# Performance work log

Measured on AMD Instinct MI355X. Metric: run time of the kernel, lower is better.

## Reference

```python
import jax, jax.numpy as jnp
import numpy as np

N = 100000      # nodes
E = 1200000     # edges
G = 2048        # graphs in batch
FIN, H, FOUT, K = 75, 16, 64, 3  # in/hidden/out channels, num_stacks


def setup_inputs() -> dict:
    key = jax.random.key(0)
    ks = jax.random.split(key, 12)
    s = 0.1
    return {
        "x": jax.random.normal(ks[0], (N, FIN), jnp.float32),
        "edge_index": jax.random.randint(ks[1], (2, E), 0, N),
        "batch": jnp.sort(jax.random.randint(ks[2], (N,), 0, G)),
        # ARMAConv1 (75 -> 16), shared weights across T=2 layers
        "w1_init": jax.random.normal(ks[3], (K, FIN, H), jnp.float32) * s,
        "w1_w": jax.random.normal(ks[4], (K, H, H), jnp.float32) * s,
        "w1_root": jax.random.normal(ks[5], (K, FIN, H), jnp.float32) * s,
        "w1_bias": jnp.zeros((K, 1, H), jnp.float32),
        # ARMAConv2 (16 -> 64), act=None
        "w2_init": jax.random.normal(ks[6], (K, H, FOUT), jnp.float32) * s,
        "w2_w": jax.random.normal(ks[7], (K, FOUT, FOUT), jnp.float32) * s,
        "w2_root": jax.random.normal(ks[8], (K, H, FOUT), jnp.float32) * s,
        "w2_bias": jnp.zeros((K, 1, FOUT), jnp.float32),
        # gather head Linear(64, 1)
        "wg": jax.random.normal(ks[9], (FOUT, 1), jnp.float32) * s,
        "bg": jnp.zeros((1,), jnp.float32),
    }


def reference(x, edge_index, batch, w1_init, w1_w, w1_root, w1_bias,
              w2_init, w2_w, w2_root, w2_bias, wg, bg):
    row, col = edge_index[0], edge_index[1]
    # gcn_norm without self-loops: deg over target nodes, sym normalization
    deg = jnp.zeros((N,), x.dtype).at[col].add(1.0)
    dinv = jnp.where(deg > 0, deg ** -0.5, 0.0)
    norm = dinv[row] * dinv[col]  # [E]

    def prop(h):  # h: [K, N, F] -> A_norm @ h per stack
        msg = h[:, row, :] * norm[None, :, None]        # [K, E, F]
        return jnp.zeros_like(h).at[:, col, :].add(msg)

    def arma(x0, wi, ww, wr, b, act):
        # x0: [N, Fin]; T=2 layers, shared weights
        out = None
        for t in range(2):
            if t == 0:
                out = jnp.einsum('nf,kfo->kno', x0, wi)   # init transform
            else:
                out = jnp.einsum('kno,kop->knp', out, ww)  # shared weight
            out = prop(out)
            out = out + jnp.einsum('nf,kfo->kno', x0, wr) + b  # root + bias
            if act:
                out = jax.nn.relu(out)
        return out.mean(axis=0)  # average over K stacks -> [N, F]

    h1 = jax.nn.relu(arma(x, w1_init, w1_w, w1_root, w1_bias, True))
    h2 = arma(h1, w2_init, w2_w, w2_root, w2_bias, False)
    # global_add_pool over graph ids, then linear head
    pooled = jnp.zeros((G, h2.shape[-1]), h2.dtype).at[batch].add(h2)
    return pooled @ wg + bg  # [G, 1]
```

## Files before the change

kernel.cpp:

```cpp
#include <hip/hip_runtime.h>

#define NN 100000
#define NE 1200000
#define NG 2048
#define NBK 391
#define CAPQ 4096
#define CAPE 5120

static inline int cdiv(long long a, int b) { return (int)((a + b - 1) / b); }

__device__ __forceinline__ unsigned short f2bf(float f) {
    unsigned int u = __float_as_uint(f);
    u += 0x7fffu + ((u >> 16) & 1u);
    return (unsigned short)(u >> 16);
}
__device__ __forceinline__ unsigned int pack2(float a, float b) {
    return (unsigned int)f2bf(a) | ((unsigned int)f2bf(b) << 16);
}
__device__ __forceinline__ float lo2f(unsigned int w) { return __uint_as_float(w << 16); }
__device__ __forceinline__ float hi2f(unsigned int w) { return __uint_as_float(w & 0xffff0000u); }

__global__ void k_init(int* __restrict__ gcur, uint4* __restrict__ A16,
                       uint4* __restrict__ B16, uint4* __restrict__ h1p16,
                       uint4* __restrict__ g1p16, float* __restrict__ dinv) {
    int g = blockIdx.x * blockDim.x + threadIdx.x;
    if (g < NBK) gcur[g] = g * CAPQ;
    if (g == NBK) dinv[NN] = 0.f;
    uint4 z = make_uint4(0u, 0u, 0u, 0u);
    int s = g - 512;
    if (s >= 0 && s < 6) {
        A16[(size_t)NN * 6 + s] = z;
        B16[(size_t)NN * 6 + s] = z;
    } else if (s >= 6 && s < 8) {
        h1p16[(size_t)NN * 2 + (s - 6)] = z;
        g1p16[(size_t)NN * 2 + (s - 6)] = z;
    }
}

__global__ __launch_bounds__(256) void k_part(const int4* __restrict__ row4,
                                              const int4* __restrict__ col4,
                                              int* __restrict__ gcur,
                                              int* __restrict__ pairs, int E4) {
    __shared__ int hcnt[NBK];
    __shared__ int hbase[NBK];
    int chunk = (E4 + gridDim.x - 1) / gridDim.x;
    int beg = blockIdx.x * chunk;
    int end = min(E4, beg + chunk);
    for (int j = threadIdx.x; j < NBK; j += 256) hcnt[j] = 0;
    __syncthreads();
    for (int g = beg + threadIdx.x; g < end; g += 256) {
        int4 c = col4[g];
        atomicAdd(&hcnt[c.x >> 8], 1);
        atomicAdd(&hcnt[c.y >> 8], 1);
        atomicAdd(&hcnt[c.z >> 8], 1);
        atomicAdd(&hcnt[c.w >> 8], 1);
    }
    __syncthreads();
    for (int j = threadIdx.x; j < NBK; j += 256) {
        int c = hcnt[j];
        hbase[j] = c > 0 ? atomicAdd(&gcur[j], c) : 0;
        hcnt[j] = 0;
    }
    __syncthreads();
    for (int g = beg + threadIdx.x; g < end; g += 256) {
        int4 c = col4[g];
        int4 r = row4[g];
        int b0 = c.x >> 8, b1 = c.y >> 8, b2 = c.z >> 8, b3 = c.w >> 8;
        int p0 = hbase[b0] + atomicAdd(&hcnt[b0], 1);
        if (p0 < (b0 + 1) * CAPQ) pairs[p0] = ((c.x & 255) << 17) | r.x;
        int p1 = hbase[b1] + atomicAdd(&hcnt[b1], 1);
        if (p1 < (b1 + 1) * CAPQ) pairs[p1] = ((c.y & 255) << 17) | r.y;
        int p2 = hbase[b2] + atomicAdd(&hcnt[b2], 1);
        if (p2 < (b2 + 1) * CAPQ) pairs[p2] = ((c.z & 255) << 17) | r.z;
        int p3 = hbase[b3] + atomicAdd(&hcnt[b3], 1);
        if (p3 < (b3 + 1) * CAPQ) pairs[p3] = ((c.w & 255) << 17) | r.w;
    }
}

__global__ __launch_bounds__(256) void k_bucket(const int* __restrict__ pairs,
                                                const int* __restrict__ gcur,
                                                int* __restrict__ esrc,
                                                int* __restrict__ rowptrp,
                                                float* __restrict__ dinv, int N) {
    __shared__ int stage[CAPE];
    __shared__ int lcnt[256];
    __shared__ int s[256];
    __shared__ int tot;
    int b = blockIdx.x;
    int base = b << 8;
    int nn = min(256, N - base);
    int qb = b * CAPQ;
    int qe = min(gcur[b], qb + CAPQ);
    int cnt = qe - qb;
    int n4 = cnt >> 2, tail = cnt & 3;
    const int4* pairs4 = (const int4*)(pairs + qb);
    int tid = threadIdx.x;
    lcnt[tid] = 0;
    __syncthreads();
    for (int g = tid; g < n4; g += 256) {
        int4 v = pairs4[g];
        atomicAdd(&lcnt[v.x >> 17], 1);
        atomicAdd(&lcnt[v.y >> 17], 1);
        atomicAdd(&lcnt[v.z >> 17], 1);
        atomicAdd(&lcnt[v.w >> 17], 1);
    }
    if (tid < tail) atomicAdd(&lcnt[pairs[qb + n4 * 4 + tid] >> 17], 1);
    __syncthreads();
    int c = lcnt[tid];
    int pc = (c + 3) & ~3;
    s[tid] = pc;
    __syncthreads();
    for (int off = 1; off < 256; off <<= 1) {
        int t = (tid >= off) ? s[tid - off] : 0;
        __syncthreads();
        s[tid] += t;
        __syncthreads();
    }
    int myofs = s[tid] - pc;
    if (tid == 255) tot = s[255];
    __syncthreads();
    int padded = tot;
    if (tid < nn) {
        dinv[base + tid] = c > 0 ? rsqrtf((float)c) : 0.f;
        rowptrp[base + tid] = ((b * CAPE + myofs) >> 2) | ((pc >> 2) << 20);
    }
    int4* stage4 = (int4*)stage;
    int pad4 = padded >> 2;
    int4 sent = make_int4(N, N, N, N);
    for (int i = tid; i < pad4; i += 256) stage4[i] = sent;
    lcnt[tid] = myofs;
    __syncthreads();
    for (int g = tid; g < n4; g += 256) {
        int4 v = pairs4[g];
        int pos;
        pos = atomicAdd(&lcnt[v.x >> 17], 1); stage[pos] = v.x & 0x1FFFF;
        pos = atomicAdd(&lcnt[v.y >> 17], 1); stage[pos] = v.y & 0x1FFFF;
        pos = atomicAdd(&lcnt[v.z >> 17], 1); stage[pos] = v.z & 0x1FFFF;
        pos = atomicAdd(&lcnt[v.w >> 17], 1); stage[pos] = v.w & 0x1FFFF;
    }
    if (tid < tail) {
        int v = pairs[qb + n4 * 4 + tid];
        int pos = atomicAdd(&lcnt[v >> 17], 1);
        stage[pos] = v & 0x1FFFF;
    }
    __syncthreads();
    int4* esrc4 = (int4*)(esrc + b * CAPE);
    for (int i = tid; i < pad4; i += 256) esrc4[i] = stage4[i];
}

__global__ void k_mmAR(const float* __restrict__ x,
                       const float* __restrict__ w1i, const float* __restrict__ w1r,
                       const float* __restrict__ b1, const float* __restrict__ dinv,
                       ushort4* __restrict__ A16s, float4* __restrict__ R4, int N) {
    __shared__ float4 Wi[900];
    __shared__ float4 Wr[900];
    __shared__ float4 Bs[12];
    const float4* wi4 = (const float4*)w1i;
    const float4* wr4 = (const float4*)w1r;
    for (int i = threadIdx.x; i < 900; i += blockDim.x) { Wi[i] = wi4[i]; Wr[i] = wr4[i]; }
    if (threadIdx.x < 12) Bs[threadIdx.x] = ((const float4*)b1)[threadIdx.x];
    __syncthreads();
    const int total = N * 12;
    const int stride = gridDim.x * blockDim.x;
    for (int idx = blockIdx.x * blockDim.x + threadIdx.x; idx < total; idx += stride) {
        int n = idx / 12;
        int q = idx - n * 12;
        int k = q >> 2, o4 = q & 3;
        const float* xp = x + (size_t)n * 75;
        const float4* wpi = Wi + (k * 75) * 4 + o4;
        const float4* wpr = Wr + (k * 75) * 4 + o4;
        float aix = 0.f, aiy = 0.f, aiz = 0.f, aiw = 0.f;
        float4 br = Bs[q];
        float arx = br.x, ary = br.y, arz = br.z, arw = br.w;
#pragma unroll
        for (int f = 0; f < 75; ++f) {
            float xv = xp[f];
            float4 wi = wpi[f * 4];
            float4 wr = wpr[f * 4];
            aix = fmaf(xv, wi.x, aix);
            aiy = fmaf(xv, wi.y, aiy);
            aiz = fmaf(xv, wi.z, aiz);
            aiw = fmaf(xv, wi.w, aiw);
            arx = fmaf(xv, wr.x, arx);
            ary = fmaf(xv, wr.y, ary);
            arz = fmaf(xv, wr.z, arz);
            arw = fmaf(xv, wr.w, arw);
        }
        float dn = dinv[n];
        ushort4 sa;
        sa.x = f2bf(aix * dn); sa.y = f2bf(aiy * dn);
        sa.z = f2bf(aiz * dn); sa.w = f2bf(aiw * dn);
        A16s[(size_t)n * 12 + q] = sa;
        R4[idx] = make_float4(arx, ary, arz, arw);
    }
}

#define ACC8(W)                                                     \
    a0 += lo2f(W.x); a1 += hi2f(W.x); a2 += lo2f(W.y); a3 += hi2f(W.y); \
    a4 += lo2f(W.z); a5 += hi2f(W.z); a6 += lo2f(W.w); a7 += hi2f(W.w);

template <int HAS_R, int COMPUTE_S, int SCALE_OUT>
__global__ void k_prop48(const uint4* __restrict__ src, const float4* __restrict__ R4,
                         const int* __restrict__ rowptrp, const int* __restrict__ esrc,
                         const float* __restrict__ dinv, float* __restrict__ sv,
                         uint4* __restrict__ dst, int N) {
    const int total = N * 6;
    const int stride = gridDim.x * blockDim.x;
    for (int idx = blockIdx.x * blockDim.x + threadIdx.x; idx < total; idx += stride) {
        int n = idx / 6;
        int q = idx - n * 6;
        int rp = rowptrp[n];
        int beg = (rp & 0xFFFFF) << 2;
        int end = beg + ((rp >> 20) << 2);
        float a0 = 0.f, a1 = 0.f, a2 = 0.f, a3 = 0.f, a4 = 0.f, a5 = 0.f, a6 = 0.f, a7 = 0.f;
        float sd = 0.f;
        int p = beg;
        for (; p + 8 <= end; p += 8) {
            int4 e0 = *(const int4*)(esrc + p);
            int4 e1 = *(const int4*)(esrc + p + 4);
            uint4 w0 = src[(size_t)e0.x * 6 + q];
            uint4 w1 = src[(size_t)e0.y * 6 + q];
            uint4 w2 = src[(size_t)e0.z * 6 + q];
            uint4 w3 = src[(size_t)e0.w * 6 + q];
            uint4 w4 = src[(size_t)e1.x * 6 + q];
            uint4 w5 = src[(size_t)e1.y * 6 + q];
            uint4 w6 = src[(size_t)e1.z * 6 + q];
            uint4 w7 = src[(size_t)e1.w * 6 + q];
            ACC8(w0); ACC8(w1); ACC8(w2); ACC8(w3);
            ACC8(w4); ACC8(w5); ACC8(w6); ACC8(w7);
            if (COMPUTE_S) {
                if (q == 0)
                    sd += ((dinv[e0.x] + dinv[e0.y]) + (dinv[e0.z] + dinv[e0.w]))
                        + ((dinv[e1.x] + dinv[e1.y]) + (dinv[e1.z] + dinv[e1.w]));
            }
        }
        if (p < end) {
            int4 e = *(const int4*)(esrc + p);
            uint4 w0 = src[(size_t)e.x * 6 + q];
            uint4 w1 = src[(size_t)e.y * 6 + q];
            uint4 w2 = src[(size_t)e.z * 6 + q];
            uint4 w3 = src[(size_t)e.w * 6 + q];
            ACC8(w0); ACC8(w1); ACC8(w2); ACC8(w3);
            if (COMPUTE_S) {
                if (q == 0)
                    sd += (dinv[e.x] + dinv[e.y]) + (dinv[e.z] + dinv[e.w]);
            }
        }
        float dn = dinv[n];
        float v0 = a0 * dn, v1 = a1 * dn, v2 = a2 * dn, v3 = a3 * dn;
        float v4 = a4 * dn, v5 = a5 * dn, v6 = a6 * dn, v7 = a7 * dn;
        if (HAS_R) {
            float4 r0 = R4[(size_t)n * 12 + q * 2];
            float4 r1 = R4[(size_t)n * 12 + q * 2 + 1];
            v0 = fmaxf(v0 + r0.x, 0.f); v1 = fmaxf(v1 + r0.y, 0.f);
            v2 = fmaxf(v2 + r0.z, 0.f); v3 = fmaxf(v3 + r0.w, 0.f);
            v4 = fmaxf(v4 + r1.x, 0.f); v5 = fmaxf(v5 + r1.y, 0.f);
            v6 = fmaxf(v6 + r1.z, 0.f); v7 = fmaxf(v7 + r1.w, 0.f);
        }
        if (SCALE_OUT) {
            v0 *= dn; v1 *= dn; v2 *= dn; v3 *= dn;
            v4 *= dn; v5 *= dn; v6 *= dn; v7 *= dn;
        }
        uint4 o;
        o.x = pack2(v0, v1); o.y = pack2(v2, v3);
        o.z = pack2(v4, v5); o.w = pack2(v6, v7);
        dst[(size_t)n * 6 + q] = o;
        if (COMPUTE_S) {
            if (q == 0) sv[n] = sd * dn;
        }
    }
}

__global__ void k_post1(const uint4* __restrict__ A16, const float4* __restrict__ R4,
                        const float* __restrict__ w1w, const float* __restrict__ dinv,
                        const float* __restrict__ u,
                        ushort4* __restrict__ h1p16s, float* __restrict__ z0, int N) {
    __shared__ float4 Ws[192];
    const float4* w4 = (const float4*)w1w;
    for (int i = threadIdx.x; i < 192; i += blockDim.x) Ws[i] = w4[i];
    __syncthreads();
    const int total = N * 4;
    const int stride = gridDim.x * blockDim.x;
    for (int idx = blockIdx.x * blockDim.x + threadIdx.x; idx < total; idx += stride) {
        int n = idx >> 2;
        int o4 = idx & 3;
        const uint4* ap = A16 + (size_t)n * 6;
        float av[48];
#pragma unroll
        for (int c6 = 0; c6 < 6; ++c6) {
            uint4 w = ap[c6];
            av[c6 * 8 + 0] = lo2f(w.x); av[c6 * 8 + 1] = hi2f(w.x);
            av[c6 * 8 + 2] = lo2f(w.y); av[c6 * 8 + 3] = hi2f(w.y);
            av[c6 * 8 + 4] = lo2f(w.z); av[c6 * 8 + 5] = hi2f(w.z);
            av[c6 * 8 + 6] = lo2f(w.w); av[c6 * 8 + 7] = hi2f(w.w);
        }
        float4 sum = make_float4(0.f, 0.f, 0.f, 0.f);
#pragma unroll
        for (int k = 0; k < 3; ++k) {
            float4 d = R4[(size_t)n * 12 + k * 4 + o4];
#pragma unroll
            for (int i = 0; i < 16; ++i) {
                float a = av[k * 16 + i];
                float4 w = Ws[(k * 16 + i) * 4 + o4];
                d.x = fmaf(a, w.x, d.x);
                d.y = fmaf(a, w.y, d.y);
                d.z = fmaf(a, w.z, d.z);
                d.w = fmaf(a, w.w, d.w);
            }
            d.x = fmaxf(d.x, 0.f); d.y = fmaxf(d.y, 0.f);
            d.z = fmaxf(d.z, 0.f); d.w = fmaxf(d.w, 0.f);
            sum.x += d.x; sum.y += d.y; sum.z += d.z; sum.w += d.w;
        }
        const float third = 1.0f / 3.0f;
        sum.x *= third; sum.y *= third; sum.z *= third; sum.w *= third;
        float dn = dinv[n];
        ushort4 sp;
        sp.x = f2bf(sum.x * dn); sp.y = f2bf(sum.y * dn);
        sp.z = f2bf(sum.z * dn); sp.w = f2bf(sum.w * dn);
        h1p16s[(size_t)n * 4 + o4] = sp;
        float4 u0q = ((const float4*)u)[o4];
        float part = sum.x * u0q.x + sum.y * u0q.y + sum.z * u0q.z + sum.w * u0q.w;
        part += __shfl_down(part, 2, 4);
        part += __shfl_down(part, 1, 4);
        if (o4 == 0) z0[n] = part;
    }
}

#define COMB8()                                                        \
    a0 += __shfl_down(a0, 4, 8); a1 += __shfl_down(a1, 4, 8);          \
    a2 += __shfl_down(a2, 4, 8); a3 += __shfl_down(a3, 4, 8);          \
    a4 += __shfl_down(a4, 4, 8); a5 += __shfl_down(a5, 4, 8);          \
    a6 += __shfl_down(a6, 4, 8); a7 += __shfl_down(a7, 4, 8);          \
    a0 += __shfl_down(a0, 2, 8); a1 += __shfl_down(a1, 2, 8);          \
    a2 += __shfl_down(a2, 2, 8); a3 += __shfl_down(a3, 2, 8);          \
    a4 += __shfl_down(a4, 2, 8); a5 += __shfl_down(a5, 2, 8);          \
    a6 += __shfl_down(a6, 2, 8); a7 += __shfl_down(a7, 2, 8);

__global__ void k_prop16z(const uint4* __restrict__ h1p16,
                          const int* __restrict__ rowptrp, const int* __restrict__ esrc,
                          const float* __restrict__ dinv, const float* __restrict__ u,
                          uint4* __restrict__ g1p16, float* __restrict__ z1, int N) {
    const int total = N * 8;
    const int stride = gridDim.x * blockDim.x;
    for (int idx = blockIdx.x * blockDim.x + threadIdx.x; idx < total; idx += stride) {
        int n = idx >> 3;
        int r = idx & 7;
        int q = r & 1;
        int es = r >> 1;
        int rp = rowptrp[n];
        int beg = ((rp & 0xFFFFF) << 2) + es * 4;
        int end = ((rp & 0xFFFFF) << 2) + ((rp >> 20) << 2);
        float a0 = 0.f, a1 = 0.f, a2 = 0.f, a3 = 0.f, a4 = 0.f, a5 = 0.f, a6 = 0.f, a7 = 0.f;
        for (int p = beg; p < end; p += 16) {
            int4 e = *(const int4*)(esrc + p);
            uint4 w0 = h1p16[(size_t)e.x * 2 + q];
            uint4 w1 = h1p16[(size_t)e.y * 2 + q];
            uint4 w2 = h1p16[(size_t)e.z * 2 + q];
            uint4 w3 = h1p16[(size_t)e.w * 2 + q];
            ACC8(w0); ACC8(w1); ACC8(w2); ACC8(w3);
        }
        COMB8();
        float dn = dinv[n];
        float v0 = a0 * dn, v1 = a1 * dn, v2 = a2 * dn, v3 = a3 * dn;
        float v4 = a4 * dn, v5 = a5 * dn, v6 = a6 * dn, v7 = a7 * dn;
        const float4* u4 = (const float4*)(u + 16);
        float4 ua = u4[q * 2], ub = u4[q * 2 + 1];
        float part = v0 * ua.x + v1 * ua.y + v2 * ua.z + v3 * ua.w
                   + v4 * ub.x + v5 * ub.y + v6 * ub.z + v7 * ub.w;
        part += __shfl_down(part, 1, 8);
        if (r == 0) z1[n] = part;
        if (r < 2) {
            uint4 o;
            o.x = pack2(v0 * dn, v1 * dn); o.y = pack2(v2 * dn, v3 * dn);
            o.z = pack2(v4 * dn, v5 * dn); o.w = pack2(v6 * dn, v7 * dn);
            g1p16[(size_t)n * 2 + q] = o;
        }
    }
}

__global__ void k_score(const uint4* __restrict__ g1p16,
                        const int* __restrict__ rowptrp, const int* __restrict__ esrc,
                        const float* __restrict__ dinv, const float* __restrict__ u,
                        const float* __restrict__ z0, const float* __restrict__ z1,
                        const float* __restrict__ sv, const int* __restrict__ batch,
                        float* __restrict__ out, int N) {
    const int total = N * 8;
    const int stride = gridDim.x * blockDim.x;
    for (int idx = blockIdx.x * blockDim.x + threadIdx.x; idx < total; idx += stride) {
        int n = idx >> 3;
        int r = idx & 7;
        int q = r & 1;
        int es = r >> 1;
        int rp = rowptrp[n];
        int beg = ((rp & 0xFFFFF) << 2) + es * 4;
        int end = ((rp & 0xFFFFF) << 2) + ((rp >> 20) << 2);
        float a0 = 0.f, a1 = 0.f, a2 = 0.f, a3 = 0.f, a4 = 0.f, a5 = 0.f, a6 = 0.f, a7 = 0.f;
        for (int p = beg; p < end; p += 16) {
            int4 e = *(const int4*)(esrc + p);
            uint4 w0 = g1p16[(size_t)e.x * 2 + q];
            uint4 w1 = g1p16[(size_t)e.y * 2 + q];
            uint4 w2 = g1p16[(size_t)e.z * 2 + q];
            uint4 w3 = g1p16[(size_t)e.w * 2 + q];
            ACC8(w0); ACC8(w1); ACC8(w2); ACC8(w3);
        }
        COMB8();
        float dn = dinv[n];
        const float4* u4 = (const float4*)(u + 32);
        float4 ua = u4[q * 2], ub = u4[q * 2 + 1];
        float part = (a0 * dn) * ua.x + (a1 * dn) * ua.y + (a2 * dn) * ua.z + (a3 * dn) * ua.w
                   + (a4 * dn) * ub.x + (a5 * dn) * ub.y + (a6 * dn) * ub.z + (a7 * dn) * ub.w;
        part += __shfl_down(part, 1, 8);
        if (r == 0) {
            float v = part + z0[n] + z1[n] + sv[n] * u[48] + u[49];
            atomicAdd(&out[batch[n]], v);
        }
    }
}

__global__ void k_comb(const float* __restrict__ w2i, const float* __restrict__ w2w,
                       const float* __restrict__ w2r, const float* __restrict__ b2,
                       const float* __restrict__ wg, const float* __restrict__ bg,
                       float* __restrict__ u, float* __restrict__ out) {
    if (blockIdx.x > 0) {
        int g = (blockIdx.x - 1) * 256 + threadIdx.x;
        if (g < NG) out[g] = bg[0];
        return;
    }
    __shared__ float t[3][64];
    int tid = threadIdx.x;
    if (tid < 64) {
#pragma unroll
        for (int k = 0; k < 3; ++k) {
            float a = 0.f;
            for (int j = 0; j < 64; ++j) a = fmaf(w2w[k * 4096 + tid * 64 + j], wg[j], a);
            t[k][tid] = a;
        }
    }
    __syncthreads();
    if (tid < 64) {
        float wgv = wg[tid];
        float tk0 = t[0][tid], tk1 = t[1][tid], tk2 = t[2][tid];
        const float third = 1.0f / 3.0f;
        for (int j = 0; j < 16; ++j) {
            float wi0 = w2i[j * 64 + tid], wi1 = w2i[1024 + j * 64 + tid], wi2 = w2i[2048 + j * 64 + tid];
            float wr0 = w2r[j * 64 + tid], wr1 = w2r[1024 + j * 64 + tid], wr2 = w2r[2048 + j * 64 + tid];
            float a2 = wi0 * tk0 + wi1 * tk1 + wi2 * tk2;
            float a1 = wr0 * tk0 + wr1 * tk1 + wr2 * tk2;
            float a0 = (wr0 + wr1 + wr2) * wgv;
#pragma unroll
            for (int off = 32; off > 0; off >>= 1) {
                a2 += __shfl_down(a2, off, 64);
                a1 += __shfl_down(a1, off, 64);
                a0 += __shfl_down(a0, off, 64);
            }
            if (tid == 0) {
                u[j] = a0 * third;
                u[16 + j] = a1 * third;
                u[32 + j] = a2 * third;
            }
        }
        float b0 = b2[tid], b1v = b2[64 + tid], b2v = b2[128 + tid];
        float c0 = b0 * tk0 + b1v * tk1 + b2v * tk2;
        float c1 = (b0 + b1v + b2v) * wgv;
#pragma unroll
        for (int off = 32; off > 0; off >>= 1) {
            c0 += __shfl_down(c0, off, 64);
            c1 += __shfl_down(c1, off, 64);
        }
        if (tid == 0) {
            u[48] = c0 * third;
            u[49] = c1 * third;
        }
    }
}

extern "C" void kernel_launch(void* const* d_in, const int* in_sizes, int n_in,
                              void* d_out, int out_size, void* d_ws, size_t ws_size,
                              hipStream_t stream) {
    const float* x   = (const float*)d_in[0];
    const int*   ei  = (const int*)d_in[1];
    const int*   batch = (const int*)d_in[2];
    const float* w1i = (const float*)d_in[3];
    const float* w1w = (const float*)d_in[4];
    const float* w1r = (const float*)d_in[5];
    const float* w1b = (const float*)d_in[6];
    const float* w2i = (const float*)d_in[7];
    const float* w2w = (const float*)d_in[8];
    const float* w2r = (const float*)d_in[9];
    const float* w2b = (const float*)d_in[10];
    const float* wg  = (const float*)d_in[11];
    const float* bg  = (const float*)d_in[12];
    float* out = (float*)d_out;

    uint4* A16   = (uint4*)d_ws;
    uint4* B16   = A16 + (size_t)(NN + 1) * 6;
    float* R     = (float*)(B16 + (size_t)(NN + 1) * 6);
    uint4* h1p16 = (uint4*)(R + (size_t)NN * 48);
    uint4* g1p16 = h1p16 + (size_t)(NN + 1) * 2;
    float* dinv  = (float*)(g1p16 + (size_t)(NN + 1) * 2);
    float* sv    = dinv + 100004;
    float* z0    = sv + NN;
    float* z1    = z0 + NN;
    float* u     = z1 + NN;
    int*   rowptrp = (int*)(u + 64);
    int*   gcur  = rowptrp + NN;
    int*   pairs = gcur + 512;
    int*   esrc  = pairs + (size_t)(NBK + 1) * CAPQ;

    const int T = 256;

    k_init<<<3, T, 0, stream>>>(gcur, A16, B16, h1p16, g1p16, dinv);
    k_part<<<512, T, 0, stream>>>((const int4*)ei, (const int4*)(ei + NE),
                                  gcur, pairs, NE / 4);
    k_bucket<<<NBK, T, 0, stream>>>(pairs, gcur, esrc, rowptrp, dinv, NN);

    k_comb<<<9, T, 0, stream>>>(w2i, w2w, w2r, w2b, wg, bg, u, out);

    k_mmAR<<<2048, T, 0, stream>>>(x, w1i, w1r, w1b, dinv, (ushort4*)A16, (float4*)R, NN);

    k_prop48<1, 1, 1><<<cdiv((long long)NN * 6, T), T, 0, stream>>>(
        A16, (const float4*)R, rowptrp, esrc, dinv, sv, B16, NN);
    k_prop48<0, 0, 0><<<cdiv((long long)NN * 6, T), T, 0, stream>>>(
        B16, nullptr, rowptrp, esrc, dinv, nullptr, A16, NN);
    k_post1<<<cdiv((long long)NN * 4, T), T, 0, stream>>>(
        A16, (const float4*)R, w1w, dinv, u, (ushort4*)h1p16, z0, NN);

    k_prop16z<<<cdiv((long long)NN * 8, T), T, 0, stream>>>(
        h1p16, rowptrp, esrc, dinv, u, g1p16, z1, NN);
    k_score<<<cdiv((long long)NN * 8, T), T, 0, stream>>>(
        g1p16, rowptrp, esrc, dinv, u, z0, z1, sv, batch, out, NN);
}
```

Baseline: 213.3 us.

## Project second-layer features to scalars before propagation, replacing 16-wide gathers

Since the second ARMA layer and the linear head are linear, the hidden features are dotted with precomputed head vectors u before propagation instead of after. Each node then carries two scalars (s12) and later one (t2) through the two graph propagations, in place of 16-wide bf16 rows. This removes most of the gather traffic in the last two edge passes and the bf16 packing. It relies on the precomputed u vectors being exact combinations of the weights, and it gives up per-node parallelism because each node is now handled by a single thread.

```diff
diff --git a/kernel.cpp b/kernel.cpp
--- a/kernel.cpp
+++ b/kernel.cpp
@@ -21,19 +21,18 @@
 __device__ __forceinline__ float hi2f(unsigned int w) { return __uint_as_float(w & 0xffff0000u); }
 
 __global__ void k_init(int* __restrict__ gcur, uint4* __restrict__ A16,
-                       uint4* __restrict__ B16, uint4* __restrict__ h1p16,
-                       uint4* __restrict__ g1p16, float* __restrict__ dinv) {
+                       uint4* __restrict__ B16, float2* __restrict__ s12,
+                       float* __restrict__ t2, float* __restrict__ dinv) {
     int g = blockIdx.x * blockDim.x + threadIdx.x;
     if (g < NBK) gcur[g] = g * CAPQ;
     if (g == NBK) dinv[NN] = 0.f;
+    if (g == NBK + 1) s12[NN] = make_float2(0.f, 0.f);
+    if (g == NBK + 2) t2[NN] = 0.f;
     uint4 z = make_uint4(0u, 0u, 0u, 0u);
     int s = g - 512;
     if (s >= 0 && s < 6) {
         A16[(size_t)NN * 6 + s] = z;
         B16[(size_t)NN * 6 + s] = z;
-    } else if (s >= 6 && s < 8) {
-        h1p16[(size_t)NN * 2 + (s - 6)] = z;
-        g1p16[(size_t)NN * 2 + (s - 6)] = z;
     }
 }
 
@@ -274,7 +273,7 @@
 __global__ void k_post1(const uint4* __restrict__ A16, const float4* __restrict__ R4,
                         const float* __restrict__ w1w, const float* __restrict__ dinv,
                         const float* __restrict__ u,
-                        ushort4* __restrict__ h1p16s, float* __restrict__ z0, int N) {
+                        float* __restrict__ z0, float2* __restrict__ s12, int N) {
     __shared__ float4 Ws[192];
     const float4* w4 = (const float4*)w1w;
     for (int i = threadIdx.x; i < 192; i += blockDim.x) Ws[i] = w4[i];
@@ -313,108 +312,77 @@
         }
         const float third = 1.0f / 3.0f;
         sum.x *= third; sum.y *= third; sum.z *= third; sum.w *= third;
-        float dn = dinv[n];
-        ushort4 sp;
-        sp.x = f2bf(sum.x * dn); sp.y = f2bf(sum.y * dn);
-        sp.z = f2bf(sum.z * dn); sp.w = f2bf(sum.w * dn);
-        h1p16s[(size_t)n * 4 + o4] = sp;
         float4 u0q = ((const float4*)u)[o4];
-        float part = sum.x * u0q.x + sum.y * u0q.y + sum.z * u0q.z + sum.w * u0q.w;
-        part += __shfl_down(part, 2, 4);
-        part += __shfl_down(part, 1, 4);
-        if (o4 == 0) z0[n] = part;
-    }
-}
-
-#define COMB8()                                                        \
-    a0 += __shfl_down(a0, 4, 8); a1 += __shfl_down(a1, 4, 8);          \
-    a2 += __shfl_down(a2, 4, 8); a3 += __shfl_down(a3, 4, 8);          \
-    a4 += __shfl_down(a4, 4, 8); a5 += __shfl_down(a5, 4, 8);          \
-    a6 += __shfl_down(a6, 4, 8); a7 += __shfl_down(a7, 4, 8);          \
-    a0 += __shfl_down(a0, 2, 8); a1 += __shfl_down(a1, 2, 8);          \
-    a2 += __shfl_down(a2, 2, 8); a3 += __shfl_down(a3, 2, 8);          \
-    a4 += __shfl_down(a4, 2, 8); a5 += __shfl_down(a5, 2, 8);          \
-    a6 += __shfl_down(a6, 2, 8); a7 += __shfl_down(a7, 2, 8);
-
-__global__ void k_prop16z(const uint4* __restrict__ h1p16,
-                          const int* __restrict__ rowptrp, const int* __restrict__ esrc,
-                          const float* __restrict__ dinv, const float* __restrict__ u,
-                          uint4* __restrict__ g1p16, float* __restrict__ z1, int N) {
-    const int total = N * 8;
-    const int stride = gridDim.x * blockDim.x;
-    for (int idx = blockIdx.x * blockDim.x + threadIdx.x; idx < total; idx += stride) {
-        int n = idx >> 3;
-        int r = idx & 7;
-        int q = r & 1;
-        int es = r >> 1;
-        int rp = rowptrp[n];
-        int beg = ((rp & 0xFFFFF) << 2) + es * 4;
-        int end = ((rp & 0xFFFFF) << 2) + ((rp >> 20) << 2);
-        float a0 = 0.f, a1 = 0.f, a2 = 0.f, a3 = 0.f, a4 = 0.f, a5 = 0.f, a6 = 0.f, a7 = 0.f;
-        for (int p = beg; p < end; p += 16) {
-            int4 e = *(const int4*)(esrc + p);
-            uint4 w0 = h1p16[(size_t)e.x * 2 + q];
-            uint4 w1 = h1p16[(size_t)e.y * 2 + q];
-            uint4 w2 = h1p16[(size_t)e.z * 2 + q];
-            uint4 w3 = h1p16[(size_t)e.w * 2 + q];
-            ACC8(w0); ACC8(w1); ACC8(w2); ACC8(w3);
-        }
-        COMB8();
-        float dn = dinv[n];
-        float v0 = a0 * dn, v1 = a1 * dn, v2 = a2 * dn, v3 = a3 * dn;
-        float v4 = a4 * dn, v5 = a5 * dn, v6 = a6 * dn, v7 = a7 * dn;
-        const float4* u4 = (const float4*)(u + 16);
-        float4 ua = u4[q * 2], ub = u4[q * 2 + 1];
-        float part = v0 * ua.x + v1 * ua.y + v2 * ua.z + v3 * ua.w
-                   + v4 * ub.x + v5 * ub.y + v6 * ub.z + v7 * ub.w;
-        part += __shfl_down(part, 1, 8);
-        if (r == 0) z1[n] = part;
-        if (r < 2) {
-            uint4 o;
-            o.x = pack2(v0 * dn, v1 * dn); o.y = pack2(v2 * dn, v3 * dn);
-            o.z = pack2(v4 * dn, v5 * dn); o.w = pack2(v6 * dn, v7 * dn);
-            g1p16[(size_t)n * 2 + q] = o;
-        }
-    }
-}
-
-__global__ void k_score(const uint4* __restrict__ g1p16,
+        float4 u1q = ((const float4*)u)[4 + o4];
+        float4 u2q = ((const float4*)u)[8 + o4];
+        float d0 = sum.x * u0q.x + sum.y * u0q.y + sum.z * u0q.z + sum.w * u0q.w;
+        float d1 = sum.x * u1q.x + sum.y * u1q.y + sum.z * u1q.z + sum.w * u1q.w;
+        float d2 = sum.x * u2q.x + sum.y * u2q.y + sum.z * u2q.z + sum.w * u2q.w;
+        d0 += __shfl_down(d0, 2, 4); d0 += __shfl_down(d0, 1, 4);
+        d1 += __shfl_down(d1, 2, 4); d1 += __shfl_down(d1, 1, 4);
+        d2 += __shfl_down(d2, 2, 4); d2 += __shfl_down(d2, 1, 4);
+        if (o4 == 0) {
+            float dn = dinv[n];
+            z0[n] = d0;
+            s12[n] = make_float2(d1 * dn, d2 * dn);
+        }
+    }
+}
+
+__global__ void k_passA(const float2* __restrict__ s12,
                         const int* __restrict__ rowptrp, const int* __restrict__ esrc,
-                        const float* __restrict__ dinv, const float* __restrict__ u,
-                        const float* __restrict__ z0, const float* __restrict__ z1,
-                        const float* __restrict__ sv, const int* __restrict__ batch,
-                        float* __restrict__ out, int N) {
-    const int total = N * 8;
-    const int stride = gridDim.x * blockDim.x;
-    for (int idx = blockIdx.x * blockDim.x + threadIdx.x; idx < total; idx += stride) {
-        int n = idx >> 3;
-        int r = idx & 7;
-        int q = r & 1;
-        int es = r >> 1;
-        int rp = rowptrp[n];
-        int beg = ((rp & 0xFFFFF) << 2) + es * 4;
-        int end = ((rp & 0xFFFFF) << 2) + ((rp >> 20) << 2);
-        float a0 = 0.f, a1 = 0.f, a2 = 0.f, a3 = 0.f, a4 = 0.f, a5 = 0.f, a6 = 0.f, a7 = 0.f;
-        for (int p = beg; p < end; p += 16) {
-            int4 e = *(const int4*)(esrc + p);
-            uint4 w0 = g1p16[(size_t)e.x * 2 + q];
-            uint4 w1 = g1p16[(size_t)e.y * 2 + q];
-            uint4 w2 = g1p16[(size_t)e.z * 2 + q];
-            uint4 w3 = g1p16[(size_t)e.w * 2 + q];
-            ACC8(w0); ACC8(w1); ACC8(w2); ACC8(w3);
-        }
-        COMB8();
-        float dn = dinv[n];
-        const float4* u4 = (const float4*)(u + 32);
-        float4 ua = u4[q * 2], ub = u4[q * 2 + 1];
-        float part = (a0 * dn) * ua.x + (a1 * dn) * ua.y + (a2 * dn) * ua.z + (a3 * dn) * ua.w
-                   + (a4 * dn) * ub.x + (a5 * dn) * ub.y + (a6 * dn) * ub.z + (a7 * dn) * ub.w;
-        part += __shfl_down(part, 1, 8);
-        if (r == 0) {
-            float v = part + z0[n] + z1[n] + sv[n] * u[48] + u[49];
-            atomicAdd(&out[batch[n]], v);
-        }
-    }
+                        const float* __restrict__ dinv, const float* __restrict__ z0,
+                        float* __restrict__ z01, float* __restrict__ t2, int N) {
+    int n = blockIdx.x * blockDim.x + threadIdx.x;
+    if (n >= N) return;
+    int rp = rowptrp[n];
+    int beg = (rp & 0xFFFFF) << 2;
+    int end = beg + ((rp >> 20) << 2);
+    float S1 = 0.f, S2 = 0.f;
+    int p = beg;
+    for (; p + 8 <= end; p += 8) {
+        int4 e0 = *(const int4*)(esrc + p);
+        int4 e1 = *(const int4*)(esrc + p + 4);
+        float2 v0 = s12[e0.x], v1 = s12[e0.y], v2 = s12[e0.z], v3 = s12[e0.w];
+        float2 v4 = s12[e1.x], v5 = s12[e1.y], v6 = s12[e1.z], v7 = s12[e1.w];
+        S1 += ((v0.x + v1.x) + (v2.x + v3.x)) + ((v4.x + v5.x) + (v6.x + v7.x));
+        S2 += ((v0.y + v1.y) + (v2.y + v3.y)) + ((v4.y + v5.y) + (v6.y + v7.y));
+    }
+    if (p < end) {
+        int4 e = *(const int4*)(esrc + p);
+        float2 v0 = s12[e.x], v1 = s12[e.y], v2 = s12[e.z], v3 = s12[e.w];
+        S1 += (v0.x + v1.x) + (v2.x + v3.x);
+        S2 += (v0.y + v1.y) + (v2.y + v3.y);
+    }
+    float dn = dinv[n];
+    z01[n] = z0[n] + dn * S1;
+    t2[n] = dn * dn * S2;
+}
+
+__global__ void k_passB(const float* __restrict__ t2,
+                        const int* __restrict__ rowptrp, const int* __restrict__ esrc,
+                        const float* __restrict__ dinv, const float* __restrict__ z01,
+                        const float* __restrict__ sv, const float* __restrict__ u,
+                        const int* __restrict__ batch, float* __restrict__ out, int N) {
+    int n = blockIdx.x * blockDim.x + threadIdx.x;
+    if (n >= N) return;
+    int rp = rowptrp[n];
+    int beg = (rp & 0xFFFFF) << 2;
+    int end = beg + ((rp >> 20) << 2);
+    float S = 0.f;
+    int p = beg;
+    for (; p + 8 <= end; p += 8) {
+        int4 e0 = *(const int4*)(esrc + p);
+        int4 e1 = *(const int4*)(esrc + p + 4);
+        S += ((t2[e0.x] + t2[e0.y]) + (t2[e0.z] + t2[e0.w]))
+           + ((t2[e1.x] + t2[e1.y]) + (t2[e1.z] + t2[e1.w]));
+    }
+    if (p < end) {
+        int4 e = *(const int4*)(esrc + p);
+        S += (t2[e.x] + t2[e.y]) + (t2[e.z] + t2[e.w]);
+    }
+    float v = z01[n] + dinv[n] * S + sv[n] * u[48] + u[49];
+    atomicAdd(&out[batch[n]], v);
 }
 
 __global__ void k_comb(const float* __restrict__ w2i, const float* __restrict__ w2w,
@@ -492,24 +460,24 @@
     const float* bg  = (const float*)d_in[12];
     float* out = (float*)d_out;
 
-    uint4* A16   = (uint4*)d_ws;
-    uint4* B16   = A16 + (size_t)(NN + 1) * 6;
-    float* R     = (float*)(B16 + (size_t)(NN + 1) * 6);
-    uint4* h1p16 = (uint4*)(R + (size_t)NN * 48);
-    uint4* g1p16 = h1p16 + (size_t)(NN + 1) * 2;
-    float* dinv  = (float*)(g1p16 + (size_t)(NN + 1) * 2);
-    float* sv    = dinv + 100004;
-    float* z0    = sv + NN;
-    float* z1    = z0 + NN;
-    float* u     = z1 + NN;
-    int*   rowptrp = (int*)(u + 64);
-    int*   gcur  = rowptrp + NN;
-    int*   pairs = gcur + 512;
-    int*   esrc  = pairs + (size_t)(NBK + 1) * CAPQ;
+    uint4*  A16  = (uint4*)d_ws;
+    uint4*  B16  = A16 + (size_t)(NN + 1) * 6;
+    float*  R    = (float*)(B16 + (size_t)(NN + 1) * 6);
+    float2* s12  = (float2*)(R + (size_t)NN * 48);
+    float*  t2   = (float*)(s12 + NN + 1);
+    float*  z0   = t2 + NN + 1;
+    float*  z01  = z0 + NN;
+    float*  dinv = z01 + NN;
+    float*  sv   = dinv + NN + 1;
+    float*  u    = sv + NN;
+    int* rowptrp = (int*)(u + 64);
+    int* gcur    = rowptrp + NN;
+    int* pairs   = gcur + 512;
+    int* esrc    = pairs + (size_t)(NBK + 1) * CAPQ;
 
     const int T = 256;
 
-    k_init<<<3, T, 0, stream>>>(gcur, A16, B16, h1p16, g1p16, dinv);
+    k_init<<<3, T, 0, stream>>>(gcur, A16, B16, s12, t2, dinv);
     k_part<<<512, T, 0, stream>>>((const int4*)ei, (const int4*)(ei + NE),
                                   gcur, pairs, NE / 4);
     k_bucket<<<NBK, T, 0, stream>>>(pairs, gcur, esrc, rowptrp, dinv, NN);
@@ -523,10 +491,8 @@
     k_prop48<0, 0, 0><<<cdiv((long long)NN * 6, T), T, 0, stream>>>(
         B16, nullptr, rowptrp, esrc, dinv, nullptr, A16, NN);
     k_post1<<<cdiv((long long)NN * 4, T), T, 0, stream>>>(
-        A16, (const float4*)R, w1w, dinv, u, (ushort4*)h1p16, z0, NN);
-
-    k_prop16z<<<cdiv((long long)NN * 8, T), T, 0, stream>>>(
-        h1p16, rowptrp, esrc, dinv, u, g1p16, z1, NN);
-    k_score<<<cdiv((long long)NN * 8, T), T, 0, stream>>>(
-        g1p16, rowptrp, esrc, dinv, u, z0, z1, sv, batch, out, NN);
-}
+        A16, (const float4*)R, w1w, dinv, u, z0, s12, NN);
+
+    k_passA<<<cdiv(NN, T), T, 0, stream>>>(s12, rowptrp, esrc, dinv, z0, z01, t2, NN);
+    k_passB<<<cdiv(NN, T), T, 0, stream>>>(t2, rowptrp, esrc, dinv, z01, sv, u, batch, out, NN);
+}
```

Measured after the change: 203.0 us. 4.9% less time.
